# Performance work log

Measured on AMD Instinct MI355X. Metric: run time of the kernel, lower is better.

## Reference

```python
import jax, jax.numpy as jnp
import numpy as np

B, S, D, H, P = 4, 4096, 1024, 8, 32
K = D // H  # head_dim = 128


def setup_inputs() -> dict:
    key = jax.random.key(0)
    ks = jax.random.split(key, 12)
    f = lambda k, shape, s: jax.random.normal(k, shape, dtype=jnp.float32) * s
    return {
        "x": f(ks[0], (B, S, D), 1.0),
        "W_proj": f(ks[1], (H, K, D), 0.03),
        "resonance_freqs": f(ks[2], (H, K), 0.01),
        "pol_W": f(ks[3], (H, P, K), 0.08),
        "pol_b": jnp.zeros((H, P), jnp.float32),
        "imp_W1": f(ks[4], (16, 1), 0.5),               # Linear(1, 16)
        "imp_b1": jnp.zeros((16,), jnp.float32),
        "imp_W2": f(ks[5], (1, 16), 0.25),              # Linear(16, 1)
        "imp_b2": jnp.zeros((1,), jnp.float32),
        "out_W": f(ks[6], (D, D), 0.03),                # Linear(dim, dim)
        "out_b": jnp.zeros((D,), jnp.float32),
        "ln_g": jnp.ones((D,), jnp.float32),
        "ln_b": jnp.zeros((D,), jnp.float32),
        "causal": 1,
    }


def reference(x, W_proj, resonance_freqs, pol_W, pol_b, imp_W1, imp_b1,
              imp_W2, imp_b2, out_W, out_b, ln_g, ln_b, causal):
    Bx, Sx, Dx = x.shape
    nH = W_proj.shape[0]
    # per-head projection + resonance frequency modulation -> (B, H, S, K)
    heads = jnp.einsum('bsd,hkd->bhsk', x, W_proj)
    heads = heads * jnp.cos(resonance_freqs * jnp.pi)[None, :, None, :]

    # --- GuaXiangDuiChong: learned cross-head impedance ---
    summary = heads.mean(axis=2)                                   # (B, H, K)
    pol = jnp.tanh(jnp.einsum('bhk,hpk->bhp', summary, pol_W) + pol_b[None])
    pol = pol / jnp.maximum(jnp.linalg.norm(pol, axis=-1, keepdims=True), 1e-12)
    dots = jnp.einsum('bhp,bgp->bhg', pol, pol)                    # (B, H, H)
    z = dots[..., None]                                            # (B, H, H, 1)
    hid = jax.nn.gelu(z * imp_W1[:, 0] + imp_b1, approximate=False)  # (B, H, H, 16)
    imp = jax.nn.softplus(jnp.einsum('bijc,oc->bijo', hid, imp_W2) + imp_b2)[..., 0]
    eye = jnp.eye(nH, dtype=x.dtype)
    impedance = imp * (1.0 - eye)                                  # (B, H, H)

    # --- cross-head transfer ---
    # h_i += sum_{j != i} heads_j / (1 + imp[i,j]) * 0.1, causally mean-masked.
    coef = (0.1 / (1.0 + impedance)) * (1.0 - eye)                 # zero diagonal (i == j skipped)
    transfer = jnp.einsum('bij,bjsk->bisk', coef, heads)           # (B, H, S, K)
    if causal and Sx > 1:
        # masked_fill(t>s)+mean over t of a key-independent tensor == scale by (s+1)/S
        scale = (jnp.arange(Sx, dtype=x.dtype) + 1.0) / Sx
        transfer = transfer * scale[None, None, :, None]
    out_heads = heads + transfer

    merged = out_heads.transpose(0, 2, 1, 3).reshape(Bx, Sx, Dx)   # cat heads on last dim
    y = merged @ out_W.T + out_b + x                               # dropout is identity in eval
    mu = y.mean(-1, keepdims=True)
    var = ((y - mu) ** 2).mean(-1, keepdims=True)
    normed = (y - mu) / jnp.sqrt(var + 1e-5) * ln_g + ln_b
    return normed, impedance
```

## Files before the change

kernel.cpp:

```cpp
#include <hip/hip_runtime.h>

typedef __bf16 bf16x8 __attribute__((ext_vector_type(8)));
typedef float f32x4 __attribute__((ext_vector_type(4)));

#define PI_F 3.14159265358979323846f

__device__ __forceinline__ unsigned short f2bf(float f) {
    unsigned u = __float_as_uint(f);
    u += 0x7FFFu + ((u >> 16) & 1u);
    return (unsigned short)(u >> 16);
}
__device__ __forceinline__ float bf2f(unsigned short h) {
    return __uint_as_float(((unsigned)h) << 16);
}

__device__ __forceinline__ void async16(const void* g, void* l) {
    __builtin_amdgcn_global_load_lds(
        (const __attribute__((address_space(1))) unsigned int*)g,
        (__attribute__((address_space(3))) unsigned int*)l, 16, 0, 0);
}

__global__ __launch_bounds__(256) void prep_w1(const float* __restrict__ W,
                                               const float* __restrict__ fr,
                                               unsigned short* __restrict__ W1b) {
    int idx = blockIdx.x * 256 + threadIdx.x;
    int n = idx >> 10, d = idx & 1023;
    int k = n >> 3, h = n & 7;
    float c = cosf(fr[h * 128 + k] * PI_F);
    W1b[idx] = f2bf(W[((h * 128 + k) << 10) + d] * c);
}

__global__ __launch_bounds__(256) void prep_wo(const float* __restrict__ Wo,
                                               unsigned short* __restrict__ Wob) {
    int idx = blockIdx.x * 256 + threadIdx.x;
    int n = idx >> 10, dp = idx & 1023;
    int k = dp >> 3, h = dp & 7;
    Wob[idx] = f2bf(Wo[(n << 10) + h * 128 + k]);
}

__global__ __launch_bounds__(256) void xbar_cast(const float* __restrict__ x,
                                                 unsigned short* __restrict__ xb,
                                                 float* __restrict__ xbar) {
    int bid = blockIdx.x;
    int b = bid >> 7;
    int s0 = (bid & 127) * 32;
    int t = threadIdx.x;
    float a0 = 0.f, a1 = 0.f, a2 = 0.f, a3 = 0.f;
    for (int i = 0; i < 32; ++i) {
        long row = (long)b * 4096 + s0 + i;
        float4 v = ((const float4*)x)[row * 256 + t];
        a0 += v.x; a1 += v.y; a2 += v.z; a3 += v.w;
        ushort4 u;
        u.x = f2bf(v.x); u.y = f2bf(v.y); u.z = f2bf(v.z); u.w = f2bf(v.w);
        ((ushort4*)xb)[row * 256 + t] = u;
    }
    float* xr = xbar + b * 1024 + t * 4;
    atomicAdd(xr + 0, a0); atomicAdd(xr + 1, a1);
    atomicAdd(xr + 2, a2); atomicAdd(xr + 3, a3);
}

__global__ __launch_bounds__(256) void summary_k(const float* __restrict__ xbar,
                                                 const float* __restrict__ W,
                                                 const float* __restrict__ fr,
                                                 float* __restrict__ summary) {
    int wave = (blockIdx.x * 256 + threadIdx.x) >> 6;
    int lane = threadIdx.x & 63;
    int b = wave >> 10, hk = wave & 1023;
    int h = hk >> 7, k = hk & 127;
    const float* wrow = &W[(h * 128 + k) << 10];
    const float* xrow = &xbar[b << 10];
    float s = 0.f;
    for (int d = lane; d < 1024; d += 64) s += xrow[d] * wrow[d];
    for (int off = 32; off; off >>= 1) s += __shfl_down(s, off);
    if (lane == 0) {
        float c = cosf(fr[h * 128 + k] * PI_F);
        summary[wave] = s * c * (1.0f / 4096.0f);
    }
}

__global__ __launch_bounds__(256) void imp_k(const float* __restrict__ summary,
                                             const float* __restrict__ pol_W,
                                             const float* __restrict__ pol_b,
                                             const float* __restrict__ imp_W1,
                                             const float* __restrict__ imp_b1,
                                             const float* __restrict__ imp_W2,
                                             const float* __restrict__ imp_b2,
                                             float* __restrict__ coef_out,
                                             float* __restrict__ imp_out) {
    __shared__ float pol[4][8][32];
    __shared__ float rn[32];
    int t = threadIdx.x;
    for (int o = t; o < 1024; o += 256) {
        int b = o >> 8, h = (o >> 5) & 7, p = o & 31;
        const float* srow = &summary[(b * 8 + h) * 128];
        const float* wrow = &pol_W[(h * 32 + p) * 128];
        float acc = pol_b[h * 32 + p];
        for (int k = 0; k < 128; ++k) acc += srow[k] * wrow[k];
        pol[b][h][p] = tanhf(acc);
    }
    __syncthreads();
    if (t < 32) {
        int b = t >> 3, h = t & 7;
        float ss = 0.f;
        for (int p = 0; p < 32; ++p) { float v = pol[b][h][p]; ss += v * v; }
        rn[t] = 1.0f / fmaxf(sqrtf(ss), 1e-12f);
    }
    __syncthreads();
    {
        int b = t >> 6, i = (t >> 3) & 7, j = t & 7;
        float d = 0.f;
        for (int p = 0; p < 32; ++p) d += pol[b][i][p] * pol[b][j][p];
        d *= rn[b * 8 + i] * rn[b * 8 + j];
        float s = imp_b2[0];
        for (int c = 0; c < 16; ++c) {
            float z = d * imp_W1[c] + imp_b1[c];
            float gl = 0.5f * z * (1.0f + erff(z * 0.70710678118654752f));
            s += gl * imp_W2[c];
        }
        float sp = fmaxf(s, 0.0f) + log1pf(expf(-fabsf(s)));
        float impv = (i == j) ? 0.0f : sp;
        imp_out[t] = impv;
        coef_out[t] = (i == j) ? 0.0f : 0.1f / (1.0f + impv);
    }
}

__global__ __launch_bounds__(256, 3) void gemm_bt(const unsigned short* __restrict__ A,
                                                  const unsigned short* __restrict__ B,
                                                  unsigned short* __restrict__ C) {
    __shared__ unsigned short As[128 * 32];
    __shared__ unsigned short Bs[128 * 32];
    const int t = threadIdx.x;
    const int wave = t >> 6;
    const int lane = t & 63;
    const int wr = wave >> 1, wc = wave & 1;
    const long rowBase = (long)blockIdx.y * 128;
    const long colBase = (long)blockIdx.x * 128;

    const int lr = lane >> 2;
    const int lb = (lane & 3) * 16;
    const char* gA = (const char*)A + (rowBase + wave * 32 + lr) * 2048 + lb;
    const char* gB = (const char*)B + (colBase + wave * 32 + lr) * 2048 + lb;
    char* lA = (char*)As + wave * 2048;
    char* lB = (char*)Bs + wave * 2048;
    const int q = lane >> 4;
    const int c16 = lane & 15;

    f32x4 acc[4][4] = {};
    for (int kt = 0; kt < 1024; kt += 32) {
        const char* a0 = gA + kt * 2;
        const char* b0 = gB + kt * 2;
        async16(a0, lA);
        async16(a0 + 16 * 2048, lA + 1024);
        async16(b0, lB);
        async16(b0 + 16 * 2048, lB + 1024);
        __syncthreads();
        bf16x8 af[4], bfr[4];
#pragma unroll
        for (int mi = 0; mi < 4; ++mi)
            af[mi] = *(const bf16x8*)((const char*)As + ((wr * 64 + mi * 16 + c16) * 32 + q * 8) * 2);
#pragma unroll
        for (int ni = 0; ni < 4; ++ni)
            bfr[ni] = *(const bf16x8*)((const char*)Bs + ((wc * 64 + ni * 16 + c16) * 32 + q * 8) * 2);
#pragma unroll
        for (int mi = 0; mi < 4; ++mi)
#pragma unroll
            for (int ni = 0; ni < 4; ++ni)
                acc[mi][ni] = __builtin_amdgcn_mfma_f32_16x16x32_bf16(af[mi], bfr[ni], acc[mi][ni], 0, 0, 0);
        __syncthreads();
    }
#pragma unroll
    for (int mi = 0; mi < 4; ++mi) {
#pragma unroll
        for (int ni = 0; ni < 4; ++ni) {
            long col = colBase + wc * 64 + ni * 16 + c16;
            long row0 = rowBase + wr * 64 + mi * 16 + q * 4;
#pragma unroll
            for (int r = 0; r < 4; ++r)
                C[(row0 + r) * 1024 + col] = f2bf(acc[mi][ni][r]);
        }
    }
}

__global__ __launch_bounds__(256) void mix_k(const unsigned short* __restrict__ heads,
                                             const float* __restrict__ coef,
                                             const int* __restrict__ causal,
                                             unsigned short* __restrict__ merged) {
    __shared__ float cf[256];
    int t = threadIdx.x;
    cf[t] = coef[t];
    __syncthreads();
    long g = (long)blockIdx.x * 256 + t;
    long bs = g >> 7;
    int m = (int)(g & 127);
    int b = (int)(bs >> 12);
    int s = (int)(bs & 4095);
    float scale = causal[0] ? (float)(s + 1) * (1.0f / 4096.0f) : 1.0f;
    const ushort4* hp = (const ushort4*)(heads + bs * 1024 + m * 8);
    ushort4 u0 = hp[0], u1 = hp[1];
    float v[8] = {bf2f(u0.x), bf2f(u0.y), bf2f(u0.z), bf2f(u0.w),
                  bf2f(u1.x), bf2f(u1.y), bf2f(u1.z), bf2f(u1.w)};
    const float* cb = cf + b * 64;
    float o[8];
#pragma unroll
    for (int i = 0; i < 8; ++i) {
        float ts = 0.f;
#pragma unroll
        for (int j = 0; j < 8; ++j) ts += cb[i * 8 + j] * v[j];
        o[i] = v[i] + scale * ts;
    }
    ushort4 o0, o1;
    o0.x = f2bf(o[0]); o0.y = f2bf(o[1]); o0.z = f2bf(o[2]); o0.w = f2bf(o[3]);
    o1.x = f2bf(o[4]); o1.y = f2bf(o[5]); o1.z = f2bf(o[6]); o1.w = f2bf(o[7]);
    ushort4* op = (ushort4*)(merged + bs * 1024 + m * 8);
    op[0] = o0; op[1] = o1;
}

__global__ __launch_bounds__(256) void ln_k(const unsigned short* __restrict__ ypre,
                                            const float* __restrict__ x,
                                            const float* __restrict__ outb,
                                            const float* __restrict__ gam,
                                            const float* __restrict__ bet,
                                            float* __restrict__ out) {
    int row = blockIdx.x;
    int t = threadIdx.x;
    long base = (long)row * 1024 + t * 4;
    ushort4 yp = *(const ushort4*)(ypre + base);
    float4 xv = *(const float4*)(x + base);
    float4 bv = *(const float4*)(outb + t * 4);
    float y0 = bf2f(yp.x) + xv.x + bv.x;
    float y1 = bf2f(yp.y) + xv.y + bv.y;
    float y2 = bf2f(yp.z) + xv.z + bv.z;
    float y3 = bf2f(yp.w) + xv.w + bv.w;
    float s = y0 + y1 + y2 + y3;
    float ss = y0 * y0 + y1 * y1 + y2 * y2 + y3 * y3;
    for (int off = 32; off; off >>= 1) {
        s += __shfl_down(s, off);
        ss += __shfl_down(ss, off);
    }
    __shared__ float red[8];
    int wv = t >> 6, ln = t & 63;
    if (ln == 0) { red[wv] = s; red[4 + wv] = ss; }
    __syncthreads();
    if (t == 0) {
        float S1 = red[0] + red[1] + red[2] + red[3];
        float S2 = red[4] + red[5] + red[6] + red[7];
        float mu = S1 * (1.0f / 1024.0f);
        float var = S2 * (1.0f / 1024.0f) - mu * mu;
        red[0] = mu;
        red[1] = 1.0f / sqrtf(var + 1e-5f);
    }
    __syncthreads();
    float mu = red[0], rs = red[1];
    float4 gv = *(const float4*)(gam + t * 4);
    float4 bb = *(const float4*)(bet + t * 4);
    float4 o;
    o.x = (y0 - mu) * rs * gv.x + bb.x;
    o.y = (y1 - mu) * rs * gv.y + bb.y;
    o.z = (y2 - mu) * rs * gv.z + bb.z;
    o.w = (y3 - mu) * rs * gv.w + bb.w;
    *(float4*)(out + base) = o;
}

extern "C" void kernel_launch(void* const* d_in, const int* in_sizes, int n_in,
                              void* d_out, int out_size, void* d_ws, size_t ws_size,
                              hipStream_t stream) {
    const float* x       = (const float*)d_in[0];
    const float* W_proj  = (const float*)d_in[1];
    const float* freqs   = (const float*)d_in[2];
    const float* pol_W   = (const float*)d_in[3];
    const float* pol_b   = (const float*)d_in[4];
    const float* imp_W1  = (const float*)d_in[5];
    const float* imp_b1  = (const float*)d_in[6];
    const float* imp_W2  = (const float*)d_in[7];
    const float* imp_b2  = (const float*)d_in[8];
    const float* out_W   = (const float*)d_in[9];
    const float* out_b   = (const float*)d_in[10];
    const float* ln_g    = (const float*)d_in[11];
    const float* ln_b    = (const float*)d_in[12];
    const int*   causal  = (const int*)d_in[13];
    float* out = (float*)d_out;

    char* ws = (char*)d_ws;
    unsigned short* xb      = (unsigned short*)(ws + 0);
    unsigned short* heads   = (unsigned short*)(ws + 33554432);
    unsigned short* w1b     = (unsigned short*)(ws + 67108864);
    unsigned short* wob     = (unsigned short*)(ws + 69206016);
    float* xbar             = (float*)(ws + 71303168);
    float* summary          = (float*)(ws + 71319552);
    float* coef             = (float*)(ws + 71335936);
    unsigned short* merged  = xb;
    unsigned short* ypre    = heads;

    hipMemsetAsync(xbar, 0, 4096 * sizeof(float), stream);
    prep_w1<<<4096, 256, 0, stream>>>(W_proj, freqs, w1b);
    prep_wo<<<4096, 256, 0, stream>>>(out_W, wob);
    xbar_cast<<<512, 256, 0, stream>>>(x, xb, xbar);
    summary_k<<<1024, 256, 0, stream>>>(xbar, W_proj, freqs, summary);
    imp_k<<<1, 256, 0, stream>>>(summary, pol_W, pol_b, imp_W1, imp_b1,
                                 imp_W2, imp_b2, coef, out + 16777216);
    gemm_bt<<<dim3(8, 128), 256, 0, stream>>>(xb, w1b, heads);
    mix_k<<<8192, 256, 0, stream>>>(heads, coef, causal, merged);
    gemm_bt<<<dim3(8, 128), 256, 0, stream>>>(merged, wob, ypre);
    ln_k<<<16384, 256, 0, stream>>>(ypre, x, out_b, ln_g, ln_b, out);
}
```

Measured before the change: 319.9 us.

## Fuse head-mix into first GEMM epilogue, merge prep kernels, swizzle GEMM blocks

The cross-head mixing step now runs inside the first GEMM's epilogue. Each 128x128 tile covers all 8 heads for 16 k-values, so the mix is done on fp32 accumulators staged in shared memory, and the separate mix kernel with its extra read and write of the heads tensor is gone. The two weight-prep kernels are merged into one launch. The summary and polarity computation moves into a 32-block kernel, which shortens the serial single-block impedance kernel. Both GEMMs use a 1D grid mapped so that neighbouring blocks land on the same XCD for L2 reuse. In exchange the epilogue needs extra shared memory and barriers, which may lower occupancy.

```diff
diff --git a/kernel.cpp b/kernel.cpp
--- a/kernel.cpp
+++ b/kernel.cpp
@@ -2,6 +2,7 @@
 
 typedef __bf16 bf16x8 __attribute__((ext_vector_type(8)));
 typedef float f32x4 __attribute__((ext_vector_type(4)));
+typedef unsigned short us8 __attribute__((ext_vector_type(8)));
 
 #define PI_F 3.14159265358979323846f
 
@@ -20,22 +21,23 @@
         (__attribute__((address_space(3))) unsigned int*)l, 16, 0, 0);
 }
 
-__global__ __launch_bounds__(256) void prep_w1(const float* __restrict__ W,
-                                               const float* __restrict__ fr,
-                                               unsigned short* __restrict__ W1b) {
+__global__ __launch_bounds__(256) void prep_k(const float* __restrict__ W,
+                                              const float* __restrict__ fr,
+                                              const float* __restrict__ Wo,
+                                              unsigned short* __restrict__ W1b,
+                                              unsigned short* __restrict__ Wob) {
     int idx = blockIdx.x * 256 + threadIdx.x;
-    int n = idx >> 10, d = idx & 1023;
-    int k = n >> 3, h = n & 7;
-    float c = cosf(fr[h * 128 + k] * PI_F);
-    W1b[idx] = f2bf(W[((h * 128 + k) << 10) + d] * c);
-}
-
-__global__ __launch_bounds__(256) void prep_wo(const float* __restrict__ Wo,
-                                               unsigned short* __restrict__ Wob) {
-    int idx = blockIdx.x * 256 + threadIdx.x;
-    int n = idx >> 10, dp = idx & 1023;
-    int k = dp >> 3, h = dp & 7;
-    Wob[idx] = f2bf(Wo[(n << 10) + h * 128 + k]);
+    if (idx < (1 << 20)) {
+        int n = idx >> 10, d = idx & 1023;
+        int k = n >> 3, h = n & 7;
+        float c = cosf(fr[h * 128 + k] * PI_F);
+        W1b[idx] = f2bf(W[((h * 128 + k) << 10) + d] * c);
+    } else {
+        int i2 = idx - (1 << 20);
+        int n = i2 >> 10, dp = i2 & 1023;
+        int k = dp >> 3, h = dp & 7;
+        Wob[i2] = f2bf(Wo[(n << 10) + h * 128 + k]);
+    }
 }
 
 __global__ __launch_bounds__(256) void xbar_cast(const float* __restrict__ x,
@@ -59,57 +61,66 @@
     atomicAdd(xr + 2, a2); atomicAdd(xr + 3, a3);
 }
 
-__global__ __launch_bounds__(256) void summary_k(const float* __restrict__ xbar,
-                                                 const float* __restrict__ W,
-                                                 const float* __restrict__ fr,
-                                                 float* __restrict__ summary) {
-    int wave = (blockIdx.x * 256 + threadIdx.x) >> 6;
-    int lane = threadIdx.x & 63;
-    int b = wave >> 10, hk = wave & 1023;
-    int h = hk >> 7, k = hk & 127;
-    const float* wrow = &W[(h * 128 + k) << 10];
+__global__ __launch_bounds__(256) void sumpol_k(const float* __restrict__ xbar,
+                                                const float* __restrict__ W,
+                                                const float* __restrict__ fr,
+                                                const float* __restrict__ pol_W,
+                                                const float* __restrict__ pol_b,
+                                                float* __restrict__ pol_g) {
+    __shared__ float summ_s[128];
+    int blk = blockIdx.x;
+    int b = blk >> 3, h = blk & 7;
+    int t = threadIdx.x;
+    int wave = t >> 6, lane = t & 63;
     const float* xrow = &xbar[b << 10];
+    for (int k = wave; k < 128; k += 4) {
+        const float* wrow = &W[(h * 128 + k) << 10];
+        float s = 0.f;
+        for (int d = lane; d < 1024; d += 64) s += xrow[d] * wrow[d];
+        for (int off = 32; off; off >>= 1) s += __shfl_down(s, off);
+        if (lane == 0) {
+            float c = cosf(fr[h * 128 + k] * PI_F);
+            summ_s[k] = s * c * (1.0f / 4096.0f);
+        }
+    }
+    __syncthreads();
+    int p = t >> 3, sl = t & 7;
+    const float* prow = &pol_W[(h * 32 + p) * 128];
     float s = 0.f;
-    for (int d = lane; d < 1024; d += 64) s += xrow[d] * wrow[d];
-    for (int off = 32; off; off >>= 1) s += __shfl_down(s, off);
-    if (lane == 0) {
-        float c = cosf(fr[h * 128 + k] * PI_F);
-        summary[wave] = s * c * (1.0f / 4096.0f);
-    }
-}
-
-__global__ __launch_bounds__(256) void imp_k(const float* __restrict__ summary,
-                                             const float* __restrict__ pol_W,
-                                             const float* __restrict__ pol_b,
-                                             const float* __restrict__ imp_W1,
-                                             const float* __restrict__ imp_b1,
-                                             const float* __restrict__ imp_W2,
-                                             const float* __restrict__ imp_b2,
-                                             float* __restrict__ coef_out,
-                                             float* __restrict__ imp_out) {
-    __shared__ float pol[4][8][32];
+    for (int i = 0; i < 16; ++i) {
+        int k = sl * 16 + i;
+        s += summ_s[k] * prow[k];
+    }
+    s += __shfl_down(s, 4);
+    s += __shfl_down(s, 2);
+    s += __shfl_down(s, 1);
+    if (sl == 0)
+        pol_g[(b * 8 + h) * 32 + p] = tanhf(s + pol_b[h * 32 + p]);
+}
+
+__global__ __launch_bounds__(256) void imp2_k(const float* __restrict__ pol_g,
+                                              const float* __restrict__ imp_W1,
+                                              const float* __restrict__ imp_b1,
+                                              const float* __restrict__ imp_W2,
+                                              const float* __restrict__ imp_b2,
+                                              float* __restrict__ coef_out,
+                                              float* __restrict__ imp_out) {
+    __shared__ float pol[1024];
     __shared__ float rn[32];
     int t = threadIdx.x;
-    for (int o = t; o < 1024; o += 256) {
-        int b = o >> 8, h = (o >> 5) & 7, p = o & 31;
-        const float* srow = &summary[(b * 8 + h) * 128];
-        const float* wrow = &pol_W[(h * 32 + p) * 128];
-        float acc = pol_b[h * 32 + p];
-        for (int k = 0; k < 128; ++k) acc += srow[k] * wrow[k];
-        pol[b][h][p] = tanhf(acc);
-    }
+    for (int o = t; o < 1024; o += 256) pol[o] = pol_g[o];
     __syncthreads();
     if (t < 32) {
-        int b = t >> 3, h = t & 7;
         float ss = 0.f;
-        for (int p = 0; p < 32; ++p) { float v = pol[b][h][p]; ss += v * v; }
+        for (int p = 0; p < 32; ++p) { float v = pol[t * 32 + p]; ss += v * v; }
         rn[t] = 1.0f / fmaxf(sqrtf(ss), 1e-12f);
     }
     __syncthreads();
     {
         int b = t >> 6, i = (t >> 3) & 7, j = t & 7;
         float d = 0.f;
-        for (int p = 0; p < 32; ++p) d += pol[b][i][p] * pol[b][j][p];
+        for (int p = 0; p < 32; ++p)
+            d += pol[(b * 8 + i) * 32 + p] * pol[(b * 8 + j) * 32 + p];
         d *= rn[b * 8 + i] * rn[b * 8 + j];
         float s = imp_b2[0];
         for (int c = 0; c < 16; ++c) {
@@ -121,6 +132,101 @@
         float impv = (i == j) ? 0.0f : sp;
         imp_out[t] = impv;
         coef_out[t] = (i == j) ? 0.0f : 0.1f / (1.0f + impv);
+    }
+}
+
+__device__ __forceinline__ void swizzle_blk(int n, long& rowBase, long& colBase) {
+    int xcd = n & 7, s = n >> 3;
+    rowBase = (long)(xcd * 16 + (s & 15)) * 128;
+    colBase = (long)(s >> 4) * 128;
+}
+
+__global__ __launch_bounds__(256, 3) void gemm1_mix(const unsigned short* __restrict__ A,
+                                                    const unsigned short* __restrict__ B,
+                                                    const float* __restrict__ coef,
+                                                    const int* __restrict__ causal,
+                                                    unsigned short* __restrict__ C) {
+    __shared__ float mixs[64 * 132];
+    __shared__ float cfs[64];
+    unsigned short* As = (unsigned short*)mixs;
+    unsigned short* Bs = As + 4096;
+    const int t = threadIdx.x;
+    const int wave = t >> 6;
+    const int lane = t & 63;
+    const int wr = wave >> 1, wc = wave & 1;
+    long rowBase, colBase;
+    swizzle_blk(blockIdx.x, rowBase, colBase);
+    const int b = (int)(rowBase >> 12);
+    if (t < 64) cfs[t] = coef[b * 64 + t];
+    const int causalv = causal[0];
+
+    const int lr = lane >> 2;
+    const int lb = (lane & 3) * 16;
+    const char* gA = (const char*)A + (rowBase + wave * 32 + lr) * 2048 + lb;
+    const char* gB = (const char*)B + (colBase + wave * 32 + lr) * 2048 + lb;
+    char* lA = (char*)As + wave * 2048;
+    char* lB = (char*)Bs + wave * 2048;
+    const int q = lane >> 4;
+    const int c16 = lane & 15;
+
+    f32x4 acc[4][4] = {};
+    for (int kt = 0; kt < 1024; kt += 32) {
+        const char* a0 = gA + kt * 2;
+        const char* b0 = gB + kt * 2;
+        async16(a0, lA);
+        async16(a0 + 16 * 2048, lA + 1024);
+        async16(b0, lB);
+        async16(b0 + 16 * 2048, lB + 1024);
+        __syncthreads();
+        bf16x8 af[4], bfr[4];
+#pragma unroll
+        for (int mi = 0; mi < 4; ++mi)
+            af[mi] = *(const bf16x8*)((const char*)As + ((wr * 64 + mi * 16 + c16) * 32 + q * 8) * 2);
+#pragma unroll
+        for (int ni = 0; ni < 4; ++ni)
+            bfr[ni] = *(const bf16x8*)((const char*)Bs + ((wc * 64 + ni * 16 + c16) * 32 + q * 8) * 2);
+#pragma unroll
+        for (int mi = 0; mi < 4; ++mi)
+#pragma unroll
+            for (int ni = 0; ni < 4; ++ni)
+                acc[mi][ni] = __builtin_amdgcn_mfma_f32_16x16x32_bf16(af[mi], bfr[ni], acc[mi][ni], 0, 0, 0);
+        __syncthreads();
+    }
+
+#pragma unroll
+    for (int pass = 0; pass < 2; ++pass) {
+        if (wr == pass) {
+#pragma unroll
+            for (int mi = 0; mi < 4; ++mi)
+#pragma unroll
+                for (int ni = 0; ni < 4; ++ni)
+#pragma unroll
+                    for (int r = 0; r < 4; ++r)
+                        mixs[(mi * 16 + q * 4 + r) * 132 + wc * 64 + ni * 16 + c16] = acc[mi][ni][r];
+        }
+        __syncthreads();
+        long rb2 = rowBase + pass * 64;
+#pragma unroll
+        for (int it = 0; it < 4; ++it) {
+            int item = t + it * 256;
+            int r = item >> 4, kg = item & 15;
+            const float* src = mixs + r * 132 + kg * 8;
+            float v[8];
+#pragma unroll
+            for (int j = 0; j < 8; ++j) v[j] = src[j];
+            long row = rb2 + r;
+            float scale = causalv ? (float)((row & 4095) + 1) * (1.0f / 4096.0f) : 1.0f;
+            us8 o;
+#pragma unroll
+            for (int i = 0; i < 8; ++i) {
+                float ts = 0.f;
+#pragma unroll
+                for (int j = 0; j < 8; ++j) ts += cfs[i * 8 + j] * v[j];
+                o[i] = f2bf(v[i] + scale * ts);
+            }
+            *(us8*)(C + row * 1024 + colBase + kg * 8) = o;
+        }
+        __syncthreads();
     }
 }
 
@@ -133,8 +239,8 @@
     const int wave = t >> 6;
     const int lane = t & 63;
     const int wr = wave >> 1, wc = wave & 1;
-    const long rowBase = (long)blockIdx.y * 128;
-    const long colBase = (long)blockIdx.x * 128;
+    long rowBase, colBase;
+    swizzle_blk(blockIdx.x, rowBase, colBase);
 
     const int lr = lane >> 2;
     const int lb = (lane & 3) * 16;
@@ -179,40 +285,6 @@
                 C[(row0 + r) * 1024 + col] = f2bf(acc[mi][ni][r]);
         }
     }
-}
-
-__global__ __launch_bounds__(256) void mix_k(const unsigned short* __restrict__ heads,
-                                             const float* __restrict__ coef,
-                                             const int* __restrict__ causal,
-                                             unsigned short* __restrict__ merged) {
-    __shared__ float cf[256];
-    int t = threadIdx.x;
-    cf[t] = coef[t];
-    __syncthreads();
-    long g = (long)blockIdx.x * 256 + t;
-    long bs = g >> 7;
-    int m = (int)(g & 127);
-    int b = (int)(bs >> 12);
-    int s = (int)(bs & 4095);
-    float scale = causal[0] ? (float)(s + 1) * (1.0f / 4096.0f) : 1.0f;
-    const ushort4* hp = (const ushort4*)(heads + bs * 1024 + m * 8);
-    ushort4 u0 = hp[0], u1 = hp[1];
-    float v[8] = {bf2f(u0.x), bf2f(u0.y), bf2f(u0.z), bf2f(u0.w),
-                  bf2f(u1.x), bf2f(u1.y), bf2f(u1.z), bf2f(u1.w)};
-    const float* cb = cf + b * 64;
-    float o[8];
-#pragma unroll
-    for (int i = 0; i < 8; ++i) {
-        float ts = 0.f;
-#pragma unroll
-        for (int j = 0; j < 8; ++j) ts += cb[i * 8 + j] * v[j];
-        o[i] = v[i] + scale * ts;
-    }
-    ushort4 o0, o1;
-    o0.x = f2bf(o[0]); o0.y = f2bf(o[1]); o0.z = f2bf(o[2]); o0.w = f2bf(o[3]);
-    o1.x = f2bf(o[4]); o1.y = f2bf(o[5]); o1.z = f2bf(o[6]); o1.w = f2bf(o[7]);
-    ushort4* op = (ushort4*)(merged + bs * 1024 + m * 8);
-    op[0] = o0; op[1] = o1;
 }
 
 __global__ __launch_bounds__(256) void ln_k(const unsigned short* __restrict__ ypre,
@@ -282,24 +354,21 @@
 
     char* ws = (char*)d_ws;
     unsigned short* xb      = (unsigned short*)(ws + 0);
-    unsigned short* heads   = (unsigned short*)(ws + 33554432);
+    unsigned short* merged  = (unsigned short*)(ws + 33554432);
     unsigned short* w1b     = (unsigned short*)(ws + 67108864);
     unsigned short* wob     = (unsigned short*)(ws + 69206016);
     float* xbar             = (float*)(ws + 71303168);
-    float* summary          = (float*)(ws + 71319552);
-    float* coef             = (float*)(ws + 71335936);
-    unsigned short* merged  = xb;
-    unsigned short* ypre    = heads;
+    float* pol_g            = (float*)(ws + 71319552);
+    float* coef             = (float*)(ws + 71323648);
+    unsigned short* ypre    = xb;
 
     hipMemsetAsync(xbar, 0, 4096 * sizeof(float), stream);
-    prep_w1<<<4096, 256, 0, stream>>>(W_proj, freqs, w1b);
-    prep_wo<<<4096, 256, 0, stream>>>(out_W, wob);
+    prep_k<<<8192, 256, 0, stream>>>(W_proj, freqs, out_W, w1b, wob);
     xbar_cast<<<512, 256, 0, stream>>>(x, xb, xbar);
-    summary_k<<<1024, 256, 0, stream>>>(xbar, W_proj, freqs, summary);
-    imp_k<<<1, 256, 0, stream>>>(summary, pol_W, pol_b, imp_W1, imp_b1,
-                                 imp_W2, imp_b2, coef, out + 16777216);
-    gemm_bt<<<dim3(8, 128), 256, 0, stream>>>(xb, w1b, heads);
-    mix_k<<<8192, 256, 0, stream>>>(heads, coef, causal, merged);
-    gemm_bt<<<dim3(8, 128), 256, 0, stream>>>(merged, wob, ypre);
+    sumpol_k<<<32, 256, 0, stream>>>(xbar, W_proj, freqs, pol_W, pol_b, pol_g);
+    imp2_k<<<1, 256, 0, stream>>>(pol_g, imp_W1, imp_b1, imp_W2, imp_b2,
+                                  coef, out + 16777216);
+    gemm1_mix<<<1024, 256, 0, stream>>>(xb, w1b, coef, causal, merged);
+    gemm_bt<<<1024, 256, 0, stream>>>(merged, wob, ypre);
     ln_k<<<16384, 256, 0, stream>>>(ypre, x, out_b, ln_g, ln_b, out);
 }
```

After: 468.6 us. 1.46x slower.
